# Optimization experiments

Hardware: AMD Instinct MI355X
Metric: run time of the kernel (lower is better)

The kernel has to match this reference:

```python
import jax, jax.numpy as jnp
import numpy as np


def _bce_per_sample(logits, labels):
    # Stable binary_cross_entropy_with_logits, mean-reduced per sample -> [B]
    l = jnp.maximum(logits, 0.0) - logits * labels + jnp.log1p(jnp.exp(-jnp.abs(logits)))
    return l.mean(axis=(1, 2, 3))


def setup_inputs() -> dict:
    key = jax.random.key(0)
    k1, k2 = jax.random.split(key)
    inputs = jax.random.normal(k1, (32, 1, 128, 128), dtype=jnp.float32)
    targets = jax.random.uniform(k2, (32, 1, 140, 140), dtype=jnp.float32)
    return {"inputs": inputs, "targets": targets}


def reference(inputs, targets):
    B, C, N1, N2 = inputs.shape
    S1 = targets.shape[-2] - N1 + 1
    S2 = targets.shape[-1] - N2 + 1
    ii, jj = jnp.meshgrid(jnp.arange(S1), jnp.arange(S2), indexing="ij")
    offsets = jnp.stack([ii.ravel(), jj.ravel()], axis=-1)  # [S, 2], S = S1*S2

    def window(off):
        # targets[:, :, i:i+N1, j:j+N2] for one shift position
        return jax.lax.dynamic_slice(targets, (0, 0, off[0], off[1]), (B, C, N1, N2))

    # candidate_shifts: [S, B, C, N1, N2]
    windows = jax.vmap(window)(offsets)
    # patch_shift_err: [S, B]
    errs = jax.vmap(lambda w: _bce_per_sample(inputs, w))(windows)

    min_loss = errs.min(axis=0)          # [B]
    min_idx = errs.argmin(axis=0)        # [B] int
    total_loss = min_loss.sum()
    adjusted_labels = windows[min_idx, jnp.arange(B)]  # [B, C, N1, N2]
    return total_loss, adjusted_labels
```

## Files before the change

### kernel.cpp

```cpp
#include <hip/hip_runtime.h>
#include <math.h>

#define NB 32
#define N  128
#define TS 140
#define NSH1 13
#define NSH 169
#define NPIX 16384
#define TPLANE 19600

__device__ inline float waveReduceSum(float v) {
#pragma unroll
    for (int o = 32; o > 0; o >>= 1) v += __shfl_down(v, o, 64);
    return v;
}

__global__ __launch_bounds__(256) void k_self(const float* __restrict__ x,
                                              float* __restrict__ sa) {
    int b = blockIdx.x, t = threadIdx.x;
    const float* xb = x + (size_t)b * NPIX;
    float acc = 0.f;
    for (int k = t; k < NPIX / 4; k += 256) {
        float4 v = *reinterpret_cast<const float4*>(xb + k * 4);
#pragma unroll
        for (int u = 0; u < 4; u++) {
            float xv = (&v.x)[u];
            acc += fmaxf(xv, 0.f) + log1pf(__expf(-fabsf(xv)));
        }
    }
    __shared__ float red[4];
    float v = waveReduceSum(acc);
    int lane = t & 63, wid = t >> 6;
    if (lane == 0) red[wid] = v;
    __syncthreads();
    if (t == 0) sa[b] = red[0] + red[1] + red[2] + red[3];
}

__global__ __launch_bounds__(256) void k_corr(const float* __restrict__ x,
                                              const float* __restrict__ y,
                                              float* __restrict__ C) {
    int di = blockIdx.x;
    int b  = blockIdx.y;
    __shared__ float ylds[N * TS];
    const float* yb = y + (size_t)b * TPLANE + di * TS;
    int t = threadIdx.x;
    for (int k = t; k < (N * TS) / 4; k += 256) {
        reinterpret_cast<float4*>(ylds)[k] = reinterpret_cast<const float4*>(yb)[k];
    }
    __syncthreads();

    const float* xb = x + (size_t)b * NPIX;
    float acc[NSH1];
#pragma unroll
    for (int d = 0; d < NSH1; d++) acc[d] = 0.f;

    for (int k = t; k < NPIX / 4; k += 256) {
        int r = k >> 5;
        int c = (k & 31) << 2;
        float4 xv = *reinterpret_cast<const float4*>(xb + r * N + c);
        const float* yrow = ylds + r * TS + c;
        float yl[16];
#pragma unroll
        for (int q = 0; q < 4; q++) {
            float4 yv = *reinterpret_cast<const float4*>(yrow + q * 4);
            yl[q * 4 + 0] = yv.x; yl[q * 4 + 1] = yv.y;
            yl[q * 4 + 2] = yv.z; yl[q * 4 + 3] = yv.w;
        }
#pragma unroll
        for (int d = 0; d < NSH1; d++) {
            acc[d] += xv.x * yl[d] + xv.y * yl[d + 1] + xv.z * yl[d + 2] + xv.w * yl[d + 3];
        }
    }

    __shared__ float red[NSH1][4];
    int lane = t & 63, wid = t >> 6;
#pragma unroll
    for (int d = 0; d < NSH1; d++) {
        float v = waveReduceSum(acc[d]);
        if (lane == 0) red[d][wid] = v;
    }
    __syncthreads();
    if (t < NSH1) {
        C[(size_t)b * NSH + di * NSH1 + t] = red[t][0] + red[t][1] + red[t][2] + red[t][3];
    }
}

__global__ __launch_bounds__(256) void k_argmax(const float* __restrict__ C,
                                                const float* __restrict__ sa,
                                                float* __restrict__ minerr,
                                                int* __restrict__ bestIdx) {
    int b = blockIdx.x, t = threadIdx.x;
    float v = -INFINITY; int idx = 0x7fffffff;
    if (t < NSH) { v = C[(size_t)b * NSH + t]; idx = t; }
    __shared__ float sv[256];
    __shared__ int si[256];
    sv[t] = v; si[t] = idx;
    __syncthreads();
    for (int o = 128; o > 0; o >>= 1) {
        if (t < o) {
            float v2 = sv[t + o]; int i2 = si[t + o];
            if (v2 > sv[t] || (v2 == sv[t] && i2 < si[t])) { sv[t] = v2; si[t] = i2; }
        }
        __syncthreads();
    }
    if (t == 0) {
        minerr[b]  = (sa[b] - sv[0]) * (1.0f / 16384.0f);
        bestIdx[b] = si[0];
    }
}

__global__ void k_total(const float* __restrict__ minerr, float* __restrict__ out) {
    int t = threadIdx.x;
    float v = (t < NB) ? minerr[t] : 0.f;
    v = waveReduceSum(v);
    if (t == 0) out[0] = v;
}

__global__ __launch_bounds__(256) void k_gather(const float* __restrict__ y,
                                                const int* __restrict__ bestIdx,
                                                float* __restrict__ out) {
    int b = blockIdx.y;
    int idx = bestIdx[b];
    int i0 = idx / NSH1, j0 = idx % NSH1;
    int p = blockIdx.x * 256 + threadIdx.x;
    int r = p >> 7, c = p & 127;
    out[1 + (size_t)b * NPIX + p] = y[(size_t)b * TPLANE + (i0 + r) * TS + j0 + c];
}

extern "C" void kernel_launch(void* const* d_in, const int* in_sizes, int n_in,
                              void* d_out, int out_size, void* d_ws, size_t ws_size,
                              hipStream_t stream) {
    const float* x = (const float*)d_in[0];
    const float* y = (const float*)d_in[1];
    float* out = (float*)d_out;
    float* ws = (float*)d_ws;

    float* sa      = ws;
    float* C       = ws + 32;
    float* minerr  = ws + 32 + 5408;
    int*   bestIdx = (int*)(ws + 32 + 5408 + 32);

    k_self  <<<NB, 256, 0, stream>>>(x, sa);
    k_corr  <<<dim3(NSH1, NB), 256, 0, stream>>>(x, y, C);
    k_argmax<<<NB, 256, 0, stream>>>(C, sa, minerr, bestIdx);
    k_total <<<1, 64, 0, stream>>>(minerr, out);
    k_gather<<<dim3(NPIX / 256, NB), 256, 0, stream>>>(y, bestIdx, out);
}
```

Baseline: 99.11 us.

## Fuse five kernels into two: merge self-term into corr, argmax/total into gather

Cuts the launch sequence from five kernels to two. The per-sample softplus sum now runs as an extra block column of the correlation kernel. The argmax, total-loss and gather steps are merged into one output kernel. Each gather block recomputes the per-sample argmax over 169 shifts redundantly, and block (0,0) computes the total loss from per-sample maxima. This removes launch and inter-kernel dependency overhead at the cost of redundant reduction work in every output block.

```diff
diff --git a/kernel.cpp b/kernel.cpp
--- a/kernel.cpp
+++ b/kernel.cpp
@@ -15,35 +15,35 @@
     return v;
 }
 
-__global__ __launch_bounds__(256) void k_self(const float* __restrict__ x,
+__global__ __launch_bounds__(256) void k_main(const float* __restrict__ x,
+                                              const float* __restrict__ y,
+                                              float* __restrict__ C,
                                               float* __restrict__ sa) {
-    int b = blockIdx.x, t = threadIdx.x;
-    const float* xb = x + (size_t)b * NPIX;
-    float acc = 0.f;
-    for (int k = t; k < NPIX / 4; k += 256) {
-        float4 v = *reinterpret_cast<const float4*>(xb + k * 4);
-#pragma unroll
-        for (int u = 0; u < 4; u++) {
-            float xv = (&v.x)[u];
-            acc += fmaxf(xv, 0.f) + log1pf(__expf(-fabsf(xv)));
-        }
-    }
-    __shared__ float red[4];
-    float v = waveReduceSum(acc);
-    int lane = t & 63, wid = t >> 6;
-    if (lane == 0) red[wid] = v;
-    __syncthreads();
-    if (t == 0) sa[b] = red[0] + red[1] + red[2] + red[3];
-}
-
-__global__ __launch_bounds__(256) void k_corr(const float* __restrict__ x,
-                                              const float* __restrict__ y,
-                                              float* __restrict__ C) {
     int di = blockIdx.x;
     int b  = blockIdx.y;
+    int t  = threadIdx.x;
     __shared__ float ylds[N * TS];
+
+    if (di == NSH1) {
+        const float* xb = x + (size_t)b * NPIX;
+        float acc = 0.f;
+        for (int k = t; k < NPIX / 4; k += 256) {
+            float4 v = *reinterpret_cast<const float4*>(xb + k * 4);
+#pragma unroll
+            for (int u = 0; u < 4; u++) {
+                float xv = (&v.x)[u];
+                acc += fmaxf(xv, 0.f) + log1pf(__expf(-fabsf(xv)));
+            }
+        }
+        float v = waveReduceSum(acc);
+        int lane = t & 63, wid = t >> 6;
+        if (lane == 0) ylds[wid] = v;
+        __syncthreads();
+        if (t == 0) sa[b] = ylds[0] + ylds[1] + ylds[2] + ylds[3];
+        return;
+    }
+
     const float* yb = y + (size_t)b * TPLANE + di * TS;
-    int t = threadIdx.x;
     for (int k = t; k < (N * TS) / 4; k += 256) {
         reinterpret_cast<float4*>(ylds)[k] = reinterpret_cast<const float4*>(yb)[k];
     }
@@ -85,15 +85,15 @@
     }
 }
 
-__global__ __launch_bounds__(256) void k_argmax(const float* __restrict__ C,
-                                                const float* __restrict__ sa,
-                                                float* __restrict__ minerr,
-                                                int* __restrict__ bestIdx) {
-    int b = blockIdx.x, t = threadIdx.x;
+__global__ __launch_bounds__(256) void k_out(const float* __restrict__ y,
+                                             const float* __restrict__ C,
+                                             const float* __restrict__ sa,
+                                             float* __restrict__ out) {
+    int b = blockIdx.y, t = threadIdx.x;
+    __shared__ float sv[256];
+    __shared__ int   si[256];
     float v = -INFINITY; int idx = 0x7fffffff;
     if (t < NSH) { v = C[(size_t)b * NSH + t]; idx = t; }
-    __shared__ float sv[256];
-    __shared__ int si[256];
     sv[t] = v; si[t] = idx;
     __syncthreads();
     for (int o = 128; o > 0; o >>= 1) {
@@ -103,28 +103,28 @@
         }
         __syncthreads();
     }
-    if (t == 0) {
-        minerr[b]  = (sa[b] - sv[0]) * (1.0f / 16384.0f);
-        bestIdx[b] = si[0];
-    }
-}
+    int best = si[0];
+    int i0 = best / NSH1, j0 = best % NSH1;
 
-__global__ void k_total(const float* __restrict__ minerr, float* __restrict__ out) {
-    int t = threadIdx.x;
-    float v = (t < NB) ? minerr[t] : 0.f;
-    v = waveReduceSum(v);
-    if (t == 0) out[0] = v;
-}
-
-__global__ __launch_bounds__(256) void k_gather(const float* __restrict__ y,
-                                                const int* __restrict__ bestIdx,
-                                                float* __restrict__ out) {
-    int b = blockIdx.y;
-    int idx = bestIdx[b];
-    int i0 = idx / NSH1, j0 = idx % NSH1;
-    int p = blockIdx.x * 256 + threadIdx.x;
+    int p = blockIdx.x * 256 + t;
     int r = p >> 7, c = p & 127;
     out[1 + (size_t)b * NPIX + p] = y[(size_t)b * TPLANE + (i0 + r) * TS + j0 + c];
+
+    if (blockIdx.x == 0 && b == 0) {
+        int bb = t >> 3, l8 = t & 7;
+        float mx = -INFINITY;
+        for (int s = l8; s < NSH; s += 8) mx = fmaxf(mx, C[(size_t)bb * NSH + s]);
+        mx = fmaxf(mx, __shfl_xor(mx, 1, 64));
+        mx = fmaxf(mx, __shfl_xor(mx, 2, 64));
+        mx = fmaxf(mx, __shfl_xor(mx, 4, 64));
+        float contrib = (l8 == 0) ? (sa[bb] - mx) : 0.f;
+        float s = waveReduceSum(contrib);
+        __shared__ float red2[4];
+        int lane = t & 63, wid = t >> 6;
+        if (lane == 0) red2[wid] = s;
+        __syncthreads();
+        if (t == 0) out[0] = (red2[0] + red2[1] + red2[2] + red2[3]) * (1.0f / 16384.0f);
+    }
 }
 
 extern "C" void kernel_launch(void* const* d_in, const int* in_sizes, int n_in,
@@ -135,14 +135,9 @@
     float* out = (float*)d_out;
     float* ws = (float*)d_ws;
 
-    float* sa      = ws;
-    float* C       = ws + 32;
-    float* minerr  = ws + 32 + 5408;
-    int*   bestIdx = (int*)(ws + 32 + 5408 + 32);
+    float* C  = ws;
+    float* sa = ws + 5408;
 
-    k_self  <<<NB, 256, 0, stream>>>(x, sa);
-    k_corr  <<<dim3(NSH1, NB), 256, 0, stream>>>(x, y, C);
-    k_argmax<<<NB, 256, 0, stream>>>(C, sa, minerr, bestIdx);
-    k_total <<<1, 64, 0, stream>>>(minerr, out);
-    k_gather<<<dim3(NPIX / 256, NB), 256, 0, stream>>>(y, bestIdx, out);
+    k_main<<<dim3(NSH1 + 1, NB), 256, 0, stream>>>(x, y, C, sa);
+    k_out <<<dim3(NPIX / 256, NB), 256, 0, stream>>>(y, C, sa, out);
 }
```

New measurement: 83.51 us. 1.19x faster.
